# Performance work log

Hardware: AMD Instinct MI355X
Metric: run time of the kernel (lower is better)

Reference implementation:

```python
import jax, jax.numpy as jnp
import numpy as np

B, N, D, H = 256, 128, 512, 512

def setup_inputs() -> dict:
    key = jax.random.key(0)
    k1, k2, k3, k4 = jax.random.split(key, 4)
    X = jax.random.normal(k1, (B, N, D), dtype=jnp.float32)
    A = jax.random.uniform(k2, (B, N, N), dtype=jnp.float32)
    # fc: Linear(D, H) params, kaiming-uniform-ish init
    lim = 1.0 / np.sqrt(D)
    W = jax.random.uniform(k3, (H, D), minval=-lim, maxval=lim, dtype=jnp.float32)
    b = jax.random.uniform(k4, (H,), minval=-lim, maxval=lim, dtype=jnp.float32)
    ln_w = jnp.ones((H,), dtype=jnp.float32)
    ln_b = jnp.zeros((H,), dtype=jnp.float32)
    return {"X": X, "A": A, "W": W, "b": b, "ln_w": ln_w, "ln_b": ln_b}

def reference(X, A, W, b, ln_w, ln_b):
    # row-normalize adjacency: A / (sum_j A[b,i,j] + 1e-6)
    A_norm = A / (jnp.sum(A, axis=2, keepdims=True) + 1e-6)
    # aggregate neighbors: (B,N,N) @ (B,N,D) -> (B,N,D)
    X_neighbor = jnp.einsum('bnm,bmd->bnd', A_norm, X)
    X_agg = X + X_neighbor
    # linear D -> H
    X_up = jnp.einsum('bnd,hd->bnh', X_agg, W) + b
    # layernorm over last dim (eps=1e-5 matches torch default)
    mu = jnp.mean(X_up, axis=-1, keepdims=True)
    var = jnp.mean(jnp.square(X_up - mu), axis=-1, keepdims=True)
    X_ln = (X_up - mu) / jnp.sqrt(var + 1e-5) * ln_w + ln_b
    return jax.nn.sigmoid(X_ln)
```

## Files before the change

### kernel.cpp

```cpp
#include <hip/hip_runtime.h>
#include <cstdint>

#define BB 256
#define NN 128
#define DD 512
#define HH 512

typedef __attribute__((ext_vector_type(8))) short bf16x8;
typedef __attribute__((ext_vector_type(16))) float f32x16;
typedef unsigned short u16;

static __device__ __forceinline__ u16 f2bf(float f) {
    union { float f; uint32_t u; } v; v.f = f;
    uint32_t u = v.u;
    return (u16)((u + 0x7FFFu + ((u >> 16) & 1u)) >> 16);
}

static __device__ __forceinline__ void gload16(const u16* g, u16* l) {
    __builtin_amdgcn_global_load_lds((const __attribute__((address_space(1))) void*)g,
                                     (__attribute__((address_space(3))) void*)l, 16, 0, 0);
}

__global__ __launch_bounds__(256) void wconv_kernel(const float* __restrict__ W, u16* __restrict__ Wb) {
    int idx = (blockIdx.x * 256 + threadIdx.x) * 4;
    float4 v = *(const float4*)(W + idx);
    ushort4 o;
    o.x = f2bf(v.x); o.y = f2bf(v.y); o.z = f2bf(v.z); o.w = f2bf(v.w);
    *(ushort4*)(Wb + idx) = o;
}

__global__ __launch_bounds__(512) void agg_kernel(const float* __restrict__ X, const float* __restrict__ A,
                                                  u16* __restrict__ Xagg) {
    __shared__ __align__(16) char smem[163840];
    u16* Ms = (u16*)smem;
    u16* Xt = (u16*)(smem + 32768);

    const int t = threadIdx.x;
    const int lane = t & 63, w = t >> 6, l31 = lane & 31, lh = lane >> 5;
    const int batch = blockIdx.x;
    const int wm = w >> 2, wn = w & 3;

    {
        const int row = t >> 2, seg = t & 3;
        const float* Ag = A + (size_t)batch * NN * NN + row * NN + seg * 32;
        float4 a[8];
        #pragma unroll
        for (int j = 0; j < 8; ++j) a[j] = *(const float4*)(Ag + j * 4);
        float s = 0.f;
        #pragma unroll
        for (int j = 0; j < 8; ++j) s += a[j].x + a[j].y + a[j].z + a[j].w;
        s += __shfl_xor(s, 1);
        s += __shfl_xor(s, 2);
        const float inv = 1.0f / (s + 1e-6f);
        #pragma unroll
        for (int c2 = 0; c2 < 4; ++c2) {
            u16 tmp[8];
            const float* pe = (const float*)&a[c2 * 2];
            #pragma unroll
            for (int e = 0; e < 8; ++e) {
                int m = seg * 32 + c2 * 8 + e;
                tmp[e] = f2bf(pe[e] * inv + (m == row ? 1.0f : 0.0f));
            }
            int c = seg * 4 + c2;
            *(uint4*)(Ms + row * 128 + ((c ^ (row & 15)) << 3)) = *(const uint4*)tmp;
        }
    }

    {
        const float* Xg = X + (size_t)batch * NN * DD;
        #pragma unroll
        for (int it = 0; it < 32; ++it) {
            int q = it * 512 + t;
            int m = q >> 7, c4 = q & 127;
            float4 v = *(const float4*)(Xg + (size_t)m * DD + c4 * 4);
            float fv[4] = {v.x, v.y, v.z, v.w};
            #pragma unroll
            for (int j = 0; j < 4; ++j) {
                int d = c4 * 4 + j;
                Xt[d * 128 + (((m >> 3) ^ ((d >> 2) & 7)) << 3) + (m & 7)] = f2bf(fv[j]);
            }
        }
    }
    __syncthreads();

    u16* Og = Xagg + (size_t)batch * NN * DD;
    #pragma unroll
    for (int dh = 0; dh < 2; ++dh) {
        f32x16 acc1[2][2];
        #pragma unroll
        for (int fi = 0; fi < 2; ++fi)
            #pragma unroll
            for (int fd = 0; fd < 2; ++fd)
                #pragma unroll
                for (int r = 0; r < 16; ++r)
                    acc1[fi][fd][r] = 0.f;

        #pragma unroll
        for (int ksl = 0; ksl < 8; ++ksl) {
            const int kc = ksl * 2 + lh;
            bf16x8 af[2], bx[2];
            #pragma unroll
            for (int fi = 0; fi < 2; ++fi) {
                int i = wm * 64 + fi * 32 + l31;
                af[fi] = *(const bf16x8*)(Ms + i * 128 + ((kc ^ (i & 15)) << 3));
            }
            #pragma unroll
            for (int fd = 0; fd < 2; ++fd) {
                int d = dh * 256 + wn * 64 + fd * 32 + l31;
                bx[fd] = *(const bf16x8*)(Xt + d * 128 + ((kc ^ ((d >> 2) & 7)) << 3));
            }
            #pragma unroll
            for (int fi = 0; fi < 2; ++fi)
                #pragma unroll
                for (int fd = 0; fd < 2; ++fd)
                    acc1[fi][fd] = __builtin_amdgcn_mfma_f32_32x32x16_bf16(af[fi], bx[fd], acc1[fi][fd], 0, 0, 0);
        }

        #pragma unroll
        for (int fi = 0; fi < 2; ++fi)
            #pragma unroll
            for (int r = 0; r < 16; ++r) {
                int i = wm * 64 + fi * 32 + (r & 3) + 8 * (r >> 2) + 4 * lh;
                #pragma unroll
                for (int fd = 0; fd < 2; ++fd) {
                    int d = dh * 256 + wn * 64 + fd * 32 + l31;
                    Og[(size_t)i * DD + d] = f2bf(acc1[fi][fd][r]);
                }
            }
    }
}

__global__ __launch_bounds__(512, 2) void gemm_ln_kernel(const u16* __restrict__ Xagg, const u16* __restrict__ Wb,
                                                         const float* __restrict__ bias, const float* __restrict__ lnw,
                                                         const float* __restrict__ lnb, float* __restrict__ out) {
    __shared__ __align__(16) char smem[73728];
    float* Pss = (float*)smem;
    float* musig = (float*)(smem + 2048);

    const int t = threadIdx.x;
    const int lane = t & 63, w = t >> 6, l31 = lane & 31, lh = lane >> 5;
    const int wm = w >> 2, wn = w & 3;
    const size_t rb = (size_t)blockIdx.x * 64;
    const u16* Xab = Xagg + rb * DD;

    float bias_v[4], lnw_v[4], lnb_v[4];
    #pragma unroll
    for (int fh = 0; fh < 4; ++fh) {
        int h = wn * 128 + fh * 32 + l31;
        bias_v[fh] = bias[h];
        lnw_v[fh] = lnw[h];
        lnb_v[fh] = lnb[h];
    }

#define STAGE(KS, BUF)                                                               \
    {                                                                                \
        const int k0_ = (KS) * 32;                                                   \
        u16* wl_ = (u16*)(smem + (BUF) * 32768);                                     \
        u16* xal_ = (u16*)(smem + 65536 + (BUF) * 4096);                             \
        _Pragma("unroll")                                                            \
        for (int it_ = 0; it_ < 4; ++it_) {                                          \
            int q_ = it_ * 512 + t;                                                  \
            int h_ = q_ >> 2, cc_ = q_ & 3;                                          \
            gload16(Wb + (size_t)h_ * DD + k0_ + ((cc_ ^ ((h_ >> 1) & 3)) * 8),      \
                    wl_ + q_ * 8);                                                   \
        }                                                                            \
        if (t < 256) {                                                               \
            int m_ = t >> 2, cc_ = t & 3;                                            \
            gload16(Xab + (size_t)m_ * DD + k0_ + ((cc_ ^ ((m_ >> 1) & 3)) * 8),     \
                    xal_ + t * 8);                                                   \
        }                                                                            \
    }

    f32x16 acc[4];
    #pragma unroll
    for (int fh = 0; fh < 4; ++fh)
        #pragma unroll
        for (int r = 0; r < 16; ++r)
            acc[fh][r] = 0.f;

    STAGE(0, 0);
    for (int ks = 0; ks < 16; ++ks) {
        const int buf = ks & 1;
        if (ks < 15) {
            STAGE(ks + 1, buf ^ 1);
            if (t < 256) asm volatile("s_waitcnt vmcnt(5)" ::: "memory");
            else         asm volatile("s_waitcnt vmcnt(4)" ::: "memory");
        } else {
            asm volatile("s_waitcnt vmcnt(0)" ::: "memory");
        }
        __builtin_amdgcn_s_barrier();
        asm volatile("" ::: "memory");

        const u16* wl = (const u16*)(smem + buf * 32768);
        const u16* xal = (const u16*)(smem + 65536 + buf * 4096);
        #pragma unroll
        for (int s2 = 0; s2 < 2; ++s2) {
            const int kc = s2 * 2 + lh;
            const int m = wm * 32 + l31;
            bf16x8 af = *(const bf16x8*)(xal + (m * 4 + (kc ^ ((m >> 1) & 3))) * 8);
            bf16x8 bw[4];
            #pragma unroll
            for (int fh = 0; fh < 4; ++fh) {
                int h = wn * 128 + fh * 32 + l31;
                bw[fh] = *(const bf16x8*)(wl + (h * 4 + (kc ^ ((h >> 1) & 3))) * 8);
            }
            #pragma unroll
            for (int fh = 0; fh < 4; ++fh)
                acc[fh] = __builtin_amdgcn_mfma_f32_32x32x16_bf16(af, bw[fh], acc[fh], 0, 0, 0);
        }
        asm volatile("" ::: "memory");
        __builtin_amdgcn_s_barrier();
    }
#undef STAGE
    __syncthreads();

    float rs[16], rss[16];
    #pragma unroll
    for (int r = 0; r < 16; ++r) {
        float s = 0.f, ss = 0.f;
        #pragma unroll
        for (int fh = 0; fh < 4; ++fh) {
            float a = acc[fh][r] + bias_v[fh];
            acc[fh][r] = a;
            s += a; ss += a * a;
        }
        rs[r] = s; rss[r] = ss;
    }
    #pragma unroll
    for (int msk = 1; msk <= 16; msk <<= 1)
        #pragma unroll
        for (int r = 0; r < 16; ++r) {
            rs[r] += __shfl_xor(rs[r], msk);
            rss[r] += __shfl_xor(rss[r], msk);
        }
    if (l31 == 0) {
        #pragma unroll
        for (int r = 0; r < 16; ++r) {
            int rl = wm * 32 + (r & 3) + 8 * (r >> 2) + 4 * lh;
            float2 v; v.x = rs[r]; v.y = rss[r];
            *(float2*)(Pss + (wn * 64 + rl) * 2) = v;
        }
    }
    __syncthreads();
    if (t < 64) {
        float s = 0.f, ss = 0.f;
        #pragma unroll
        for (int q = 0; q < 4; ++q) {
            float2 v = *(const float2*)(Pss + (q * 64 + t) * 2);
            s += v.x; ss += v.y;
        }
        float mean = s * (1.0f / 512.0f);
        float var = ss * (1.0f / 512.0f) - mean * mean;
        float2 mz; mz.x = mean; mz.y = rsqrtf(var + 1e-5f);
        *(float2*)(musig + t * 2) = mz;
    }
    __syncthreads();

    #pragma unroll
    for (int r = 0; r < 16; ++r) {
        int rl = wm * 32 + (r & 3) + 8 * (r >> 2) + 4 * lh;
        float2 mz = *(const float2*)(musig + rl * 2);
        #pragma unroll
        for (int fh = 0; fh < 4; ++fh) {
            float xn = (acc[fh][r] - mz.x) * mz.y * lnw_v[fh] + lnb_v[fh];
            out[(rb + rl) * HH + wn * 128 + fh * 32 + l31] = 1.0f / (1.0f + __expf(-xn));
        }
    }
}

extern "C" void kernel_launch(void* const* d_in, const int* in_sizes, int n_in,
                              void* d_out, int out_size, void* d_ws, size_t ws_size,
                              hipStream_t stream) {
    const float* X = (const float*)d_in[0];
    const float* A = (const float*)d_in[1];
    const float* W = (const float*)d_in[2];
    const float* bias = (const float*)d_in[3];
    const float* lnw = (const float*)d_in[4];
    const float* lnb = (const float*)d_in[5];
    float* out = (float*)d_out;

    u16* Xagg = (u16*)d_ws;
    u16* Wb = (u16*)d_ws + (size_t)BB * NN * DD;

    hipLaunchKernelGGL(wconv_kernel, dim3(256), dim3(256), 0, stream, W, Wb);
    hipLaunchKernelGGL(agg_kernel, dim3(256), dim3(512), 0, stream, X, A, Xagg);
    hipLaunchKernelGGL(gemm_ln_kernel, dim3(512), dim3(512), 0, stream, Xagg, Wb, bias, lnw, lnb, out);
}
```

Measured before the change: 78.52 us.

## Reorder computation: apply linear projection first, then aggregate with fused layernorm

Uses associativity to compute Y = X·Wᵀ first (stored transposed in bf16), then computes (A_norm + I)·Y per batch, with bias, layernorm and sigmoid fused into the aggregation kernel. This removes the separate Xagg intermediate pass and lets the aggregation GEMM feed the epilogue directly. The projection kernel converts X to bf16 on the fly instead of reading a precomputed bf16 copy. The output of the first GEMM is rounded to bf16 before aggregation, which changes the rounding points.

```diff
diff --git a/kernel.cpp b/kernel.cpp
--- a/kernel.cpp
+++ b/kernel.cpp
@@ -29,23 +29,135 @@
     *(ushort4*)(Wb + idx) = o;
 }
 
-__global__ __launch_bounds__(512) void agg_kernel(const float* __restrict__ X, const float* __restrict__ A,
-                                                  u16* __restrict__ Xagg) {
+__global__ __launch_bounds__(512, 2) void yt_kernel(const float* __restrict__ X, const u16* __restrict__ Wb,
+                                                    u16* __restrict__ Yt) {
+    __shared__ __align__(16) char smem[49152];
+
+    const int t = threadIdx.x;
+    const int lane = t & 63, w = t >> 6, l31 = lane & 31, lh = lane >> 5;
+    const int mblk = (int)blockIdx.x >> 2, hblk = (int)blockIdx.x & 3;
+    const int m0 = mblk * 256, h0 = hblk * 128;
+    const int hq = w & 3, mh = w >> 2;
+
+    float4 xr[4];
+
+#define XLOAD(KS)                                                                         \
+    {                                                                                     \
+        const int k0_ = (KS) * 32;                                                        \
+        _Pragma("unroll")                                                                 \
+        for (int it_ = 0; it_ < 4; ++it_) {                                               \
+            int q_ = it_ * 512 + t;                                                       \
+            int m_ = q_ >> 3, c4_ = q_ & 7;                                               \
+            xr[it_] = *(const float4*)(X + (size_t)(m0 + m_) * DD + k0_ + c4_ * 4);       \
+        }                                                                                 \
+    }
+
+#define XWRITE(BUF)                                                                       \
+    {                                                                                     \
+        char* xb_ = smem + (BUF) * 16384;                                                 \
+        _Pragma("unroll")                                                                 \
+        for (int it_ = 0; it_ < 4; ++it_) {                                               \
+            int q_ = it_ * 512 + t;                                                       \
+            int m_ = q_ >> 3, c4_ = q_ & 7;                                               \
+            ushort4 o_;                                                                   \
+            o_.x = f2bf(xr[it_].x); o_.y = f2bf(xr[it_].y);                               \
+            o_.z = f2bf(xr[it_].z); o_.w = f2bf(xr[it_].w);                               \
+            *(ushort4*)(xb_ + m_ * 64 + (((c4_ >> 1) ^ (m_ & 3)) << 4) + ((c4_ & 1) << 3)) = o_; \
+        }                                                                                 \
+    }
+
+#define WGLOAD(KS, BUF)                                                                   \
+    {                                                                                     \
+        u16* wd_ = (u16*)(smem + 32768 + (BUF) * 8192);                                   \
+        int h_ = t >> 2, c_ = t & 3;                                                      \
+        gload16(Wb + (size_t)(h0 + h_) * DD + (KS) * 32 + ((c_ ^ (h_ & 3)) * 8),          \
+                wd_ + t * 8);                                                             \
+    }
+
+    f32x16 acc[4];
+    #pragma unroll
+    for (int mf = 0; mf < 4; ++mf)
+        #pragma unroll
+        for (int r = 0; r < 16; ++r)
+            acc[mf][r] = 0.f;
+
+    XLOAD(0);
+    WGLOAD(0, 0);
+    XWRITE(0);
+    __syncthreads();
+
+    for (int ks = 0; ks < 16; ++ks) {
+        const int buf = ks & 1;
+        if (ks < 15) {
+            XLOAD(ks + 1);
+            WGLOAD(ks + 1, buf ^ 1);
+        }
+        const u16* xs = (const u16*)(smem + buf * 16384);
+        const u16* ws = (const u16*)(smem + 32768 + buf * 8192);
+        #pragma unroll
+        for (int s2 = 0; s2 < 2; ++s2) {
+            const int kc = s2 * 2 + lh;
+            const int h = hq * 32 + l31;
+            bf16x8 af = *(const bf16x8*)(ws + h * 32 + ((kc ^ (h & 3)) << 3));
+            bf16x8 bx[4];
+            #pragma unroll
+            for (int mf = 0; mf < 4; ++mf) {
+                int m = mh * 128 + mf * 32 + l31;
+                bx[mf] = *(const bf16x8*)(xs + m * 32 + ((kc ^ (m & 3)) << 3));
+            }
+            #pragma unroll
+            for (int mf = 0; mf < 4; ++mf)
+                acc[mf] = __builtin_amdgcn_mfma_f32_32x32x16_bf16(af, bx[mf], acc[mf], 0, 0, 0);
+        }
+        __syncthreads();
+        if (ks < 15) XWRITE(buf ^ 1);
+        __syncthreads();
+    }
+#undef XLOAD
+#undef XWRITE
+#undef WGLOAD
+
+    #pragma unroll
+    for (int mf = 0; mf < 4; ++mf) {
+        int gm = m0 + mh * 128 + mf * 32 + l31;
+        int bt = gm >> 7, mloc = gm & 127;
+        u16* base = Yt + (size_t)bt * (HH * NN) + (size_t)h0 * NN + mloc;
+        #pragma unroll
+        for (int r = 0; r < 16; ++r) {
+            int h = hq * 32 + (r & 3) + 8 * (r >> 2) + 4 * lh;
+            base[(size_t)h * NN] = f2bf(acc[mf][r]);
+        }
+    }
+}
+
+__global__ __launch_bounds__(512) void aggln_kernel(const float* __restrict__ A, const u16* __restrict__ Yt,
+                                                    const float* __restrict__ bias, const float* __restrict__ lnw,
+                                                    const float* __restrict__ lnb, float* __restrict__ out) {
     __shared__ __align__(16) char smem[163840];
     u16* Ms = (u16*)smem;
-    u16* Xt = (u16*)(smem + 32768);
+    u16* Yl = (u16*)(smem + 32768);
 
     const int t = threadIdx.x;
     const int lane = t & 63, w = t >> 6, l31 = lane & 31, lh = lane >> 5;
     const int batch = blockIdx.x;
-    const int wm = w >> 2, wn = w & 3;
+
+    const int row = t >> 2, seg = t & 3;
+    const float* Ag = A + (size_t)batch * NN * NN + row * NN + seg * 32;
+    float4 a[8];
+    #pragma unroll
+    for (int j = 0; j < 8; ++j) a[j] = *(const float4*)(Ag + j * 4);
 
     {
-        const int row = t >> 2, seg = t & 3;
-        const float* Ag = A + (size_t)batch * NN * NN + row * NN + seg * 32;
-        float4 a[8];
-        #pragma unroll
-        for (int j = 0; j < 8; ++j) a[j] = *(const float4*)(Ag + j * 4);
+        const u16* Ytg = Yt + (size_t)batch * (HH * NN);
+        #pragma unroll
+        for (int it = 0; it < 16; ++it) {
+            int q = it * 512 + t;
+            int h = q >> 4, c = q & 15;
+            gload16(Ytg + (size_t)h * NN + ((c ^ (h & 7)) * 8), Yl + q * 8);
+        }
+    }
+
+    {
         float s = 0.f;
         #pragma unroll
         for (int j = 0; j < 8; ++j) s += a[j].x + a[j].y + a[j].z + a[j].w;
@@ -65,205 +177,96 @@
             *(uint4*)(Ms + row * 128 + ((c ^ (row & 15)) << 3)) = *(const uint4*)tmp;
         }
     }
-
-    {
-        const float* Xg = X + (size_t)batch * NN * DD;
-        #pragma unroll
-        for (int it = 0; it < 32; ++it) {
-            int q = it * 512 + t;
-            int m = q >> 7, c4 = q & 127;
-            float4 v = *(const float4*)(Xg + (size_t)m * DD + c4 * 4);
-            float fv[4] = {v.x, v.y, v.z, v.w};
-            #pragma unroll
-            for (int j = 0; j < 4; ++j) {
-                int d = c4 * 4 + j;
-                Xt[d * 128 + (((m >> 3) ^ ((d >> 2) & 7)) << 3) + (m & 7)] = f2bf(fv[j]);
-            }
-        }
-    }
     __syncthreads();
 
-    u16* Og = Xagg + (size_t)batch * NN * DD;
-    #pragma unroll
-    for (int dh = 0; dh < 2; ++dh) {
-        f32x16 acc1[2][2];
-        #pragma unroll
-        for (int fi = 0; fi < 2; ++fi)
-            #pragma unroll
-            for (int fd = 0; fd < 2; ++fd)
-                #pragma unroll
-                for (int r = 0; r < 16; ++r)
-                    acc1[fi][fd][r] = 0.f;
-
-        #pragma unroll
-        for (int ksl = 0; ksl < 8; ++ksl) {
-            const int kc = ksl * 2 + lh;
-            bf16x8 af[2], bx[2];
-            #pragma unroll
-            for (int fi = 0; fi < 2; ++fi) {
-                int i = wm * 64 + fi * 32 + l31;
-                af[fi] = *(const bf16x8*)(Ms + i * 128 + ((kc ^ (i & 15)) << 3));
-            }
-            #pragma unroll
-            for (int fd = 0; fd < 2; ++fd) {
-                int d = dh * 256 + wn * 64 + fd * 32 + l31;
-                bx[fd] = *(const bf16x8*)(Xt + d * 128 + ((kc ^ ((d >> 2) & 7)) << 3));
-            }
-            #pragma unroll
-            for (int fi = 0; fi < 2; ++fi)
-                #pragma unroll
-                for (int fd = 0; fd < 2; ++fd)
-                    acc1[fi][fd] = __builtin_amdgcn_mfma_f32_32x32x16_bf16(af[fi], bx[fd], acc1[fi][fd], 0, 0, 0);
-        }
-
-        #pragma unroll
-        for (int fi = 0; fi < 2; ++fi)
-            #pragma unroll
-            for (int r = 0; r < 16; ++r) {
-                int i = wm * 64 + fi * 32 + (r & 3) + 8 * (r >> 2) + 4 * lh;
-                #pragma unroll
-                for (int fd = 0; fd < 2; ++fd) {
-                    int d = dh * 256 + wn * 64 + fd * 32 + l31;
-                    Og[(size_t)i * DD + d] = f2bf(acc1[fi][fd][r]);
-                }
-            }
-    }
-}
-
-__global__ __launch_bounds__(512, 2) void gemm_ln_kernel(const u16* __restrict__ Xagg, const u16* __restrict__ Wb,
-                                                         const float* __restrict__ bias, const float* __restrict__ lnw,
-                                                         const float* __restrict__ lnb, float* __restrict__ out) {
-    __shared__ __align__(16) char smem[73728];
-    float* Pss = (float*)smem;
-    float* musig = (float*)(smem + 2048);
-
-    const int t = threadIdx.x;
-    const int lane = t & 63, w = t >> 6, l31 = lane & 31, lh = lane >> 5;
-    const int wm = w >> 2, wn = w & 3;
-    const size_t rb = (size_t)blockIdx.x * 64;
-    const u16* Xab = Xagg + rb * DD;
-
-    float bias_v[4], lnw_v[4], lnb_v[4];
-    #pragma unroll
-    for (int fh = 0; fh < 4; ++fh) {
-        int h = wn * 128 + fh * 32 + l31;
+    float bias_v[2], lnw_v[2], lnb_v[2];
+    #pragma unroll
+    for (int fh = 0; fh < 2; ++fh) {
+        int h = w * 64 + fh * 32 + l31;
         bias_v[fh] = bias[h];
         lnw_v[fh] = lnw[h];
         lnb_v[fh] = lnb[h];
     }
-
-#define STAGE(KS, BUF)                                                               \
-    {                                                                                \
-        const int k0_ = (KS) * 32;                                                   \
-        u16* wl_ = (u16*)(smem + (BUF) * 32768);                                     \
-        u16* xal_ = (u16*)(smem + 65536 + (BUF) * 4096);                             \
-        _Pragma("unroll")                                                            \
-        for (int it_ = 0; it_ < 4; ++it_) {                                          \
-            int q_ = it_ * 512 + t;                                                  \
-            int h_ = q_ >> 2, cc_ = q_ & 3;                                          \
-            gload16(Wb + (size_t)h_ * DD + k0_ + ((cc_ ^ ((h_ >> 1) & 3)) * 8),      \
-                    wl_ + q_ * 8);                                                   \
-        }                                                                            \
-        if (t < 256) {                                                               \
-            int m_ = t >> 2, cc_ = t & 3;                                            \
-            gload16(Xab + (size_t)m_ * DD + k0_ + ((cc_ ^ ((m_ >> 1) & 3)) * 8),     \
-                    xal_ + t * 8);                                                   \
-        }                                                                            \
-    }
-
-    f32x16 acc[4];
-    #pragma unroll
-    for (int fh = 0; fh < 4; ++fh)
-        #pragma unroll
-        for (int r = 0; r < 16; ++r)
-            acc[fh][r] = 0.f;
-
-    STAGE(0, 0);
-    for (int ks = 0; ks < 16; ++ks) {
-        const int buf = ks & 1;
-        if (ks < 15) {
-            STAGE(ks + 1, buf ^ 1);
-            if (t < 256) asm volatile("s_waitcnt vmcnt(5)" ::: "memory");
-            else         asm volatile("s_waitcnt vmcnt(4)" ::: "memory");
-        } else {
-            asm volatile("s_waitcnt vmcnt(0)" ::: "memory");
-        }
-        __builtin_amdgcn_s_barrier();
-        asm volatile("" ::: "memory");
-
-        const u16* wl = (const u16*)(smem + buf * 32768);
-        const u16* xal = (const u16*)(smem + 65536 + buf * 4096);
-        #pragma unroll
-        for (int s2 = 0; s2 < 2; ++s2) {
-            const int kc = s2 * 2 + lh;
-            const int m = wm * 32 + l31;
-            bf16x8 af = *(const bf16x8*)(xal + (m * 4 + (kc ^ ((m >> 1) & 3))) * 8);
-            bf16x8 bw[4];
-            #pragma unroll
-            for (int fh = 0; fh < 4; ++fh) {
-                int h = wn * 128 + fh * 32 + l31;
-                bw[fh] = *(const bf16x8*)(wl + (h * 4 + (kc ^ ((h >> 1) & 3))) * 8);
-            }
-            #pragma unroll
-            for (int fh = 0; fh < 4; ++fh)
+    float* Og = out + (size_t)batch * NN * HH;
+
+    #pragma unroll
+    for (int ih = 0; ih < 4; ++ih) {
+        f32x16 acc[2];
+        #pragma unroll
+        for (int fh = 0; fh < 2; ++fh)
+            #pragma unroll
+            for (int r = 0; r < 16; ++r)
+                acc[fh][r] = 0.f;
+
+        #pragma unroll
+        for (int s8 = 0; s8 < 8; ++s8) {
+            const int kc = s8 * 2 + lh;
+            const int i = ih * 32 + l31;
+            bf16x8 af = *(const bf16x8*)(Ms + i * 128 + ((kc ^ (i & 15)) << 3));
+            bf16x8 bw[2];
+            #pragma unroll
+            for (int fh = 0; fh < 2; ++fh) {
+                int h = w * 64 + fh * 32 + l31;
+                bw[fh] = *(const bf16x8*)(Yl + h * 128 + ((kc ^ (h & 7)) << 3));
+            }
+            #pragma unroll
+            for (int fh = 0; fh < 2; ++fh)
                 acc[fh] = __builtin_amdgcn_mfma_f32_32x32x16_bf16(af, bw[fh], acc[fh], 0, 0, 0);
         }
-        asm volatile("" ::: "memory");
-        __builtin_amdgcn_s_barrier();
-    }
-#undef STAGE
-    __syncthreads();
-
-    float rs[16], rss[16];
-    #pragma unroll
-    for (int r = 0; r < 16; ++r) {
-        float s = 0.f, ss = 0.f;
-        #pragma unroll
-        for (int fh = 0; fh < 4; ++fh) {
-            float a = acc[fh][r] + bias_v[fh];
-            acc[fh][r] = a;
-            s += a; ss += a * a;
-        }
-        rs[r] = s; rss[r] = ss;
-    }
-    #pragma unroll
-    for (int msk = 1; msk <= 16; msk <<= 1)
+        __syncthreads();
+
+        float* Pss = (float*)(smem + ih * 8192);
+        float* musig = (float*)(smem + ih * 8192 + 4096);
+
+        float rs[16], rss[16];
         #pragma unroll
         for (int r = 0; r < 16; ++r) {
-            rs[r] += __shfl_xor(rs[r], msk);
-            rss[r] += __shfl_xor(rss[r], msk);
-        }
-    if (l31 == 0) {
+            float a0 = acc[0][r] + bias_v[0];
+            float a1 = acc[1][r] + bias_v[1];
+            acc[0][r] = a0; acc[1][r] = a1;
+            rs[r] = a0 + a1;
+            rss[r] = a0 * a0 + a1 * a1;
+        }
+        #pragma unroll
+        for (int msk = 1; msk <= 16; msk <<= 1)
+            #pragma unroll
+            for (int r = 0; r < 16; ++r) {
+                rs[r] += __shfl_xor(rs[r], msk);
+                rss[r] += __shfl_xor(rss[r], msk);
+            }
+        if (l31 == 0) {
+            #pragma unroll
+            for (int r = 0; r < 16; ++r) {
+                int rl = (r & 3) + 8 * (r >> 2) + 4 * lh;
+                float2 v; v.x = rs[r]; v.y = rss[r];
+                *(float2*)(Pss + (w * 32 + rl) * 2) = v;
+            }
+        }
+        __syncthreads();
+        if (t < 32) {
+            float s = 0.f, ss = 0.f;
+            #pragma unroll
+            for (int q = 0; q < 8; ++q) {
+                float2 v = *(const float2*)(Pss + (q * 32 + t) * 2);
+                s += v.x; ss += v.y;
+            }
+            float mean = s * (1.0f / 512.0f);
+            float var = ss * (1.0f / 512.0f) - mean * mean;
+            float2 mz; mz.x = mean; mz.y = rsqrtf(var + 1e-5f);
+            *(float2*)(musig + t * 2) = mz;
+        }
+        __syncthreads();
+
         #pragma unroll
         for (int r = 0; r < 16; ++r) {
-            int rl = wm * 32 + (r & 3) + 8 * (r >> 2) + 4 * lh;
-            float2 v; v.x = rs[r]; v.y = rss[r];
-            *(float2*)(Pss + (wn * 64 + rl) * 2) = v;
-        }
-    }
-    __syncthreads();
-    if (t < 64) {
-        float s = 0.f, ss = 0.f;
-        #pragma unroll
-        for (int q = 0; q < 4; ++q) {
-            float2 v = *(const float2*)(Pss + (q * 64 + t) * 2);
-            s += v.x; ss += v.y;
-        }
-        float mean = s * (1.0f / 512.0f);
-        float var = ss * (1.0f / 512.0f) - mean * mean;
-        float2 mz; mz.x = mean; mz.y = rsqrtf(var + 1e-5f);
-        *(float2*)(musig + t * 2) = mz;
-    }
-    __syncthreads();
-
-    #pragma unroll
-    for (int r = 0; r < 16; ++r) {
-        int rl = wm * 32 + (r & 3) + 8 * (r >> 2) + 4 * lh;
-        float2 mz = *(const float2*)(musig + rl * 2);
-        #pragma unroll
-        for (int fh = 0; fh < 4; ++fh) {
-            float xn = (acc[fh][r] - mz.x) * mz.y * lnw_v[fh] + lnb_v[fh];
-            out[(rb + rl) * HH + wn * 128 + fh * 32 + l31] = 1.0f / (1.0f + __expf(-xn));
+            int rl = (r & 3) + 8 * (r >> 2) + 4 * lh;
+            float2 mz = *(const float2*)(musig + rl * 2);
+            #pragma unroll
+            for (int fh = 0; fh < 2; ++fh) {
+                float xn = (acc[fh][r] - mz.x) * mz.y * lnw_v[fh] + lnb_v[fh];
+                Og[(size_t)(ih * 32 + rl) * HH + w * 64 + fh * 32 + l31] =
+                    1.0f / (1.0f + __expf(-xn));
+            }
         }
     }
 }
@@ -279,10 +282,10 @@
     const float* lnb = (const float*)d_in[5];
     float* out = (float*)d_out;
 
-    u16* Xagg = (u16*)d_ws;
-    u16* Wb = (u16*)d_ws + (size_t)BB * NN * DD;
+    u16* Yt = (u16*)d_ws;
+    u16* Wb = (u16*)d_ws + (size_t)BB * HH * NN;
 
     hipLaunchKernelGGL(wconv_kernel, dim3(256), dim3(256), 0, stream, W, Wb);
-    hipLaunchKernelGGL(agg_kernel, dim3(256), dim3(512), 0, stream, X, A, Xagg);
-    hipLaunchKernelGGL(gemm_ln_kernel, dim3(512), dim3(512), 0, stream, Xagg, Wb, bias, lnw, lnb, out);
-}
+    hipLaunchKernelGGL(yt_kernel, dim3(512), dim3(512), 0, stream, X, Wb, Yt);
+    hipLaunchKernelGGL(aggln_kernel, dim3(256), dim3(512), 0, stream, A, Yt, bias, lnw, lnb, out);
+}
```

Result: slower. 97.95 us (+24.8%).

## Halve GEMM-LN block to 4 waves, each computing a 64x128 tile

Applied to the files above, without the earlier changes.

The GEMM+LayerNorm kernel drops from 8 waves to 4 waves per block. Each wave now covers all 64 rows and 128 output columns, with two A fragments reused across four W fragments, so each wave issues more MFMAs per LDS read. The hand-tuned vmcnt waits with raw s_barrier are replaced by plain __syncthreads. That may serialise the prefetch with compute, since the barrier now waits on all outstanding loads. It also doubles accumulator registers per wave and halves the waves available to hide latency.

```diff
diff --git a/kernel.cpp b/kernel.cpp
--- a/kernel.cpp
+++ b/kernel.cpp
@@ -130,7 +130,7 @@
     }
 }
 
-__global__ __launch_bounds__(512, 2) void gemm_ln_kernel(const u16* __restrict__ Xagg, const u16* __restrict__ Wb,
+__global__ __launch_bounds__(256, 2) void gemm_ln_kernel(const u16* __restrict__ Xagg, const u16* __restrict__ Wb,
                                                          const float* __restrict__ bias, const float* __restrict__ lnw,
                                                          const float* __restrict__ lnb, float* __restrict__ out) {
     __shared__ __align__(16) char smem[73728];
@@ -139,14 +139,13 @@
 
     const int t = threadIdx.x;
     const int lane = t & 63, w = t >> 6, l31 = lane & 31, lh = lane >> 5;
-    const int wm = w >> 2, wn = w & 3;
     const size_t rb = (size_t)blockIdx.x * 64;
     const u16* Xab = Xagg + rb * DD;
 
     float bias_v[4], lnw_v[4], lnb_v[4];
     #pragma unroll
     for (int fh = 0; fh < 4; ++fh) {
-        int h = wn * 128 + fh * 32 + l31;
+        int h = w * 128 + fh * 32 + l31;
         bias_v[fh] = bias[h];
         lnw_v[fh] = lnw[h];
         lnb_v[fh] = lnb[h];
@@ -158,88 +157,92 @@
         u16* wl_ = (u16*)(smem + (BUF) * 32768);                                     \
         u16* xal_ = (u16*)(smem + 65536 + (BUF) * 4096);                             \
         _Pragma("unroll")                                                            \
-        for (int it_ = 0; it_ < 4; ++it_) {                                          \
-            int q_ = it_ * 512 + t;                                                  \
+        for (int it_ = 0; it_ < 8; ++it_) {                                          \
+            int q_ = it_ * 256 + t;                                                  \
             int h_ = q_ >> 2, cc_ = q_ & 3;                                          \
             gload16(Wb + (size_t)h_ * DD + k0_ + ((cc_ ^ ((h_ >> 1) & 3)) * 8),      \
                     wl_ + q_ * 8);                                                   \
         }                                                                            \
-        if (t < 256) {                                                               \
+        {                                                                            \
             int m_ = t >> 2, cc_ = t & 3;                                            \
             gload16(Xab + (size_t)m_ * DD + k0_ + ((cc_ ^ ((m_ >> 1) & 3)) * 8),     \
                     xal_ + t * 8);                                                   \
         }                                                                            \
     }
 
-    f32x16 acc[4];
-    #pragma unroll
-    for (int fh = 0; fh < 4; ++fh)
-        #pragma unroll
-        for (int r = 0; r < 16; ++r)
-            acc[fh][r] = 0.f;
+    f32x16 acc[2][4];
+    #pragma unroll
+    for (int mi = 0; mi < 2; ++mi)
+        #pragma unroll
+        for (int fh = 0; fh < 4; ++fh)
+            #pragma unroll
+            for (int r = 0; r < 16; ++r)
+                acc[mi][fh][r] = 0.f;
 
     STAGE(0, 0);
+    __syncthreads();
     for (int ks = 0; ks < 16; ++ks) {
         const int buf = ks & 1;
-        if (ks < 15) {
-            STAGE(ks + 1, buf ^ 1);
-            if (t < 256) asm volatile("s_waitcnt vmcnt(5)" ::: "memory");
-            else         asm volatile("s_waitcnt vmcnt(4)" ::: "memory");
-        } else {
-            asm volatile("s_waitcnt vmcnt(0)" ::: "memory");
-        }
-        __builtin_amdgcn_s_barrier();
-        asm volatile("" ::: "memory");
+        if (ks < 15) STAGE(ks + 1, buf ^ 1);
 
         const u16* wl = (const u16*)(smem + buf * 32768);
         const u16* xal = (const u16*)(smem + 65536 + buf * 4096);
         #pragma unroll
         for (int s2 = 0; s2 < 2; ++s2) {
             const int kc = s2 * 2 + lh;
-            const int m = wm * 32 + l31;
-            bf16x8 af = *(const bf16x8*)(xal + (m * 4 + (kc ^ ((m >> 1) & 3))) * 8);
-            bf16x8 bw[4];
+            bf16x8 af[2], bw[4];
+            #pragma unroll
+            for (int mi = 0; mi < 2; ++mi) {
+                int m = mi * 32 + l31;
+                af[mi] = *(const bf16x8*)(xal + (m * 4 + (kc ^ ((m >> 1) & 3))) * 8);
+            }
             #pragma unroll
             for (int fh = 0; fh < 4; ++fh) {
-                int h = wn * 128 + fh * 32 + l31;
+                int h = w * 128 + fh * 32 + l31;
                 bw[fh] = *(const bf16x8*)(wl + (h * 4 + (kc ^ ((h >> 1) & 3))) * 8);
             }
             #pragma unroll
-            for (int fh = 0; fh < 4; ++fh)
-                acc[fh] = __builtin_amdgcn_mfma_f32_32x32x16_bf16(af, bw[fh], acc[fh], 0, 0, 0);
-        }
-        asm volatile("" ::: "memory");
-        __builtin_amdgcn_s_barrier();
+            for (int mi = 0; mi < 2; ++mi)
+                #pragma unroll
+                for (int fh = 0; fh < 4; ++fh)
+                    acc[mi][fh] = __builtin_amdgcn_mfma_f32_32x32x16_bf16(af[mi], bw[fh], acc[mi][fh], 0, 0, 0);
+        }
+        __syncthreads();
     }
 #undef STAGE
-    __syncthreads();
-
-    float rs[16], rss[16];
-    #pragma unroll
-    for (int r = 0; r < 16; ++r) {
-        float s = 0.f, ss = 0.f;
-        #pragma unroll
-        for (int fh = 0; fh < 4; ++fh) {
-            float a = acc[fh][r] + bias_v[fh];
-            acc[fh][r] = a;
-            s += a; ss += a * a;
-        }
-        rs[r] = s; rss[r] = ss;
-    }
+
+    float rs[2][16], rss[2][16];
+    #pragma unroll
+    for (int mi = 0; mi < 2; ++mi)
+        #pragma unroll
+        for (int r = 0; r < 16; ++r) {
+            float s = 0.f, ss = 0.f;
+            #pragma unroll
+            for (int fh = 0; fh < 4; ++fh) {
+                float a = acc[mi][fh][r] + bias_v[fh];
+                acc[mi][fh][r] = a;
+                s += a; ss += a * a;
+            }
+            rs[mi][r] = s; rss[mi][r] = ss;
+        }
     #pragma unroll
     for (int msk = 1; msk <= 16; msk <<= 1)
         #pragma unroll
-        for (int r = 0; r < 16; ++r) {
-            rs[r] += __shfl_xor(rs[r], msk);
-            rss[r] += __shfl_xor(rss[r], msk);
-        }
+        for (int mi = 0; mi < 2; ++mi)
+            #pragma unroll
+            for (int r = 0; r < 16; ++r) {
+                rs[mi][r] += __shfl_xor(rs[mi][r], msk);
+                rss[mi][r] += __shfl_xor(rss[mi][r], msk);
+            }
     if (l31 == 0) {
         #pragma unroll
-        for (int r = 0; r < 16; ++r) {
-            int rl = wm * 32 + (r & 3) + 8 * (r >> 2) + 4 * lh;
-            float2 v; v.x = rs[r]; v.y = rss[r];
-            *(float2*)(Pss + (wn * 64 + rl) * 2) = v;
-        }
+        for (int mi = 0; mi < 2; ++mi)
+            #pragma unroll
+            for (int r = 0; r < 16; ++r) {
+                int rl = mi * 32 + (r & 3) + 8 * (r >> 2) + 4 * lh;
+                float2 v; v.x = rs[mi][r]; v.y = rss[mi][r];
+                *(float2*)(Pss + (w * 64 + rl) * 2) = v;
+            }
     }
     __syncthreads();
     if (t < 64) {
@@ -257,15 +260,17 @@
     __syncthreads();
 
     #pragma unroll
-    for (int r = 0; r < 16; ++r) {
-        int rl = wm * 32 + (r & 3) + 8 * (r >> 2) + 4 * lh;
-        float2 mz = *(const float2*)(musig + rl * 2);
-        #pragma unroll
-        for (int fh = 0; fh < 4; ++fh) {
-            float xn = (acc[fh][r] - mz.x) * mz.y * lnw_v[fh] + lnb_v[fh];
-            out[(rb + rl) * HH + wn * 128 + fh * 32 + l31] = 1.0f / (1.0f + __expf(-xn));
-        }
-    }
+    for (int mi = 0; mi < 2; ++mi)
+        #pragma unroll
+        for (int r = 0; r < 16; ++r) {
+            int rl = mi * 32 + (r & 3) + 8 * (r >> 2) + 4 * lh;
+            float2 mz = *(const float2*)(musig + rl * 2);
+            #pragma unroll
+            for (int fh = 0; fh < 4; ++fh) {
+                float xn = (acc[mi][fh][r] - mz.x) * mz.y * lnw_v[fh] + lnb_v[fh];
+                out[(rb + rl) * HH + w * 128 + fh * 32 + l31] = 1.0f / (1.0f + __expf(-xn));
+            }
+        }
 }
 
 extern "C" void kernel_launch(void* const* d_in, const int* in_sizes, int n_in,
@@ -284,5 +289,5 @@
 
     hipLaunchKernelGGL(wconv_kernel, dim3(256), dim3(256), 0, stream, W, Wb);
     hipLaunchKernelGGL(agg_kernel, dim3(256), dim3(512), 0, stream, X, A, Xagg);
-    hipLaunchKernelGGL(gemm_ln_kernel, dim3(512), dim3(512), 0, stream, Xagg, Wb, bias, lnw, lnb, out);
-}
+    hipLaunchKernelGGL(gemm_ln_kernel, dim3(512), dim3(256), 0, stream, Xagg, Wb, bias, lnw, lnb, out);
+}
```

Result: slower. 92.30 us (+17.6%).

## Shrink GEMM+LN tile to 32 rows, preload full A slab, single-buffer W

Applied to the files above, without the earlier changes.

The fused GEMM+LayerNorm kernel now uses 256-thread blocks covering 32 rows each, so twice as many blocks are launched. The whole 32x512 activation slab is loaded into LDS once with an XOR swizzle. The W tile is refilled each k-step without double buffering, behind two __syncthreads, so the overlap of loads with MFMA work is lost. Each W tile now feeds only 32 rows, which doubles total W traffic from L2 in exchange for more blocks and less LDS per block.

```diff
diff --git a/kernel.cpp b/kernel.cpp
--- a/kernel.cpp
+++ b/kernel.cpp
@@ -130,45 +130,47 @@
     }
 }
 
-__global__ __launch_bounds__(512, 2) void gemm_ln_kernel(const u16* __restrict__ Xagg, const u16* __restrict__ Wb,
+__global__ __launch_bounds__(256, 2) void gemm_ln_kernel(const u16* __restrict__ Xagg, const u16* __restrict__ Wb,
                                                          const float* __restrict__ bias, const float* __restrict__ lnw,
                                                          const float* __restrict__ lnb, float* __restrict__ out) {
-    __shared__ __align__(16) char smem[73728];
+    __shared__ __align__(16) char smem[65536];
     float* Pss = (float*)smem;
-    float* musig = (float*)(smem + 2048);
+    float* musig = (float*)(smem + 1024);
 
     const int t = threadIdx.x;
     const int lane = t & 63, w = t >> 6, l31 = lane & 31, lh = lane >> 5;
-    const int wm = w >> 2, wn = w & 3;
-    const size_t rb = (size_t)blockIdx.x * 64;
+    const size_t rb = (size_t)blockIdx.x * 32;
     const u16* Xab = Xagg + rb * DD;
 
     float bias_v[4], lnw_v[4], lnb_v[4];
     #pragma unroll
     for (int fh = 0; fh < 4; ++fh) {
-        int h = wn * 128 + fh * 32 + l31;
+        int h = w * 128 + fh * 32 + l31;
         bias_v[fh] = bias[h];
         lnw_v[fh] = lnw[h];
         lnb_v[fh] = lnb[h];
     }
 
-#define STAGE(KS, BUF)                                                               \
-    {                                                                                \
-        const int k0_ = (KS) * 32;                                                   \
-        u16* wl_ = (u16*)(smem + (BUF) * 32768);                                     \
-        u16* xal_ = (u16*)(smem + 65536 + (BUF) * 4096);                             \
-        _Pragma("unroll")                                                            \
-        for (int it_ = 0; it_ < 4; ++it_) {                                          \
-            int q_ = it_ * 512 + t;                                                  \
-            int h_ = q_ >> 2, cc_ = q_ & 3;                                          \
-            gload16(Wb + (size_t)h_ * DD + k0_ + ((cc_ ^ ((h_ >> 1) & 3)) * 8),      \
-                    wl_ + q_ * 8);                                                   \
-        }                                                                            \
-        if (t < 256) {                                                               \
-            int m_ = t >> 2, cc_ = t & 3;                                            \
-            gload16(Xab + (size_t)m_ * DD + k0_ + ((cc_ ^ ((m_ >> 1) & 3)) * 8),     \
-                    xal_ + t * 8);                                                   \
-        }                                                                            \
+#define ASTAGE                                                                        \
+    {                                                                                 \
+        _Pragma("unroll")                                                             \
+        for (int it_ = 0; it_ < 8; ++it_) {                                           \
+            int q_ = it_ * 256 + t;                                                   \
+            int m_ = q_ >> 6, cp_ = q_ & 63;                                          \
+            gload16(Xab + (size_t)m_ * DD + ((cp_ ^ (m_ & 15)) * 8),                  \
+                    (u16*)smem + q_ * 8);                                             \
+        }                                                                             \
+    }
+#define WSTAGE(KS)                                                                    \
+    {                                                                                 \
+        u16* wl_ = (u16*)(smem + 32768);                                              \
+        _Pragma("unroll")                                                             \
+        for (int it_ = 0; it_ < 8; ++it_) {                                           \
+            int q_ = it_ * 256 + t;                                                   \
+            int h_ = q_ >> 2, cc_ = q_ & 3;                                           \
+            gload16(Wb + (size_t)h_ * DD + (KS) * 32 + ((cc_ ^ ((h_ >> 1) & 3)) * 8), \
+                    wl_ + q_ * 8);                                                    \
+        }                                                                             \
     }
 
     f32x16 acc[4];
@@ -178,40 +180,36 @@
         for (int r = 0; r < 16; ++r)
             acc[fh][r] = 0.f;
 
-    STAGE(0, 0);
+    ASTAGE;
+    WSTAGE(0);
+    __syncthreads();
+
     for (int ks = 0; ks < 16; ++ks) {
-        const int buf = ks & 1;
-        if (ks < 15) {
-            STAGE(ks + 1, buf ^ 1);
-            if (t < 256) asm volatile("s_waitcnt vmcnt(5)" ::: "memory");
-            else         asm volatile("s_waitcnt vmcnt(4)" ::: "memory");
-        } else {
-            asm volatile("s_waitcnt vmcnt(0)" ::: "memory");
-        }
-        __builtin_amdgcn_s_barrier();
-        asm volatile("" ::: "memory");
-
-        const u16* wl = (const u16*)(smem + buf * 32768);
-        const u16* xal = (const u16*)(smem + 65536 + buf * 4096);
+        const u16* al = (const u16*)smem;
+        const u16* wl = (const u16*)(smem + 32768);
         #pragma unroll
         for (int s2 = 0; s2 < 2; ++s2) {
             const int kc = s2 * 2 + lh;
-            const int m = wm * 32 + l31;
-            bf16x8 af = *(const bf16x8*)(xal + (m * 4 + (kc ^ ((m >> 1) & 3))) * 8);
+            const int gc = ks * 4 + kc;
+            bf16x8 af = *(const bf16x8*)(al + (l31 * 64 + (gc ^ (l31 & 15))) * 8);
             bf16x8 bw[4];
             #pragma unroll
             for (int fh = 0; fh < 4; ++fh) {
-                int h = wn * 128 + fh * 32 + l31;
+                int h = w * 128 + fh * 32 + l31;
                 bw[fh] = *(const bf16x8*)(wl + (h * 4 + (kc ^ ((h >> 1) & 3))) * 8);
             }
             #pragma unroll
             for (int fh = 0; fh < 4; ++fh)
                 acc[fh] = __builtin_amdgcn_mfma_f32_32x32x16_bf16(af, bw[fh], acc[fh], 0, 0, 0);
         }
-        asm volatile("" ::: "memory");
-        __builtin_amdgcn_s_barrier();
-    }
-#undef STAGE
+        if (ks < 15) {
+            __syncthreads();
+            WSTAGE(ks + 1);
+            __syncthreads();
+        }
+    }
+#undef ASTAGE
+#undef WSTAGE
     __syncthreads();
 
     float rs[16], rss[16];
@@ -236,17 +234,17 @@
     if (l31 == 0) {
         #pragma unroll
         for (int r = 0; r < 16; ++r) {
-            int rl = wm * 32 + (r & 3) + 8 * (r >> 2) + 4 * lh;
+            int rl = (r & 3) + 8 * (r >> 2) + 4 * lh;
             float2 v; v.x = rs[r]; v.y = rss[r];
-            *(float2*)(Pss + (wn * 64 + rl) * 2) = v;
-        }
-    }
-    __syncthreads();
-    if (t < 64) {
+            *(float2*)(Pss + (w * 32 + rl) * 2) = v;
+        }
+    }
+    __syncthreads();
+    if (t < 32) {
         float s = 0.f, ss = 0.f;
         #pragma unroll
         for (int q = 0; q < 4; ++q) {
-            float2 v = *(const float2*)(Pss + (q * 64 + t) * 2);
+            float2 v = *(const float2*)(Pss + (q * 32 + t) * 2);
             s += v.x; ss += v.y;
         }
         float mean = s * (1.0f / 512.0f);
@@ -258,12 +256,12 @@
 
     #pragma unroll
     for (int r = 0; r < 16; ++r) {
-        int rl = wm * 32 + (r & 3) + 8 * (r >> 2) + 4 * lh;
+        int rl = (r & 3) + 8 * (r >> 2) + 4 * lh;
         float2 mz = *(const float2*)(musig + rl * 2);
         #pragma unroll
         for (int fh = 0; fh < 4; ++fh) {
             float xn = (acc[fh][r] - mz.x) * mz.y * lnw_v[fh] + lnb_v[fh];
-            out[(rb + rl) * HH + wn * 128 + fh * 32 + l31] = 1.0f / (1.0f + __expf(-xn));
+            out[(rb + rl) * HH + w * 128 + fh * 32 + l31] = 1.0f / (1.0f + __expf(-xn));
         }
     }
 }
@@ -284,5 +282,5 @@
 
     hipLaunchKernelGGL(wconv_kernel, dim3(256), dim3(256), 0, stream, W, Wb);
     hipLaunchKernelGGL(agg_kernel, dim3(256), dim3(512), 0, stream, X, A, Xagg);
-    hipLaunchKernelGGL(gemm_ln_kernel, dim3(512), dim3(512), 0, stream, Xagg, Wb, bias, lnw, lnb, out);
-}
+    hipLaunchKernelGGL(gemm_ln_kernel, dim3(1024), dim3(256), 0, stream, Xagg, Wb, bias, lnw, lnb, out);
+}
```

Result: slower. 88.16 us (+12.3%).
